# Optimization experiments

Hardware: AMD Instinct MI355X
Metric: run time of the kernel (lower is better)

Reference implementation:

```python
import jax, jax.numpy as jnp
import numpy as np

N = 96            # max_nodes == R (all nodes real)
IN_DIM, HID, ZD = 64, 256, 64
E = 1024
U = N * (N - 1) // 2
NUM_LOGITS = U + N   # 4656
MPM_ITERS = 50
BN_EPS = 1e-5

def _xavier_relu(k, fi, fo):
    # xavier_uniform with gain('relu') = sqrt(2)
    s = (2.0 ** 0.5) * (6.0 / (fi + fo)) ** 0.5
    return jax.random.uniform(k, (fi, fo), jnp.float32, -s, s)

def setup_inputs() -> dict:
    key = jax.random.key(0)
    ks = jax.random.split(key, 12)
    x = jax.random.normal(ks[0], (N, IN_DIM), jnp.float32)
    edge_index = jnp.stack([jax.random.randint(ks[1], (E,), 0, N),
                            jax.random.randint(ks[2], (E,), 0, N)]).astype(jnp.int32)
    a = (jax.random.uniform(ks[3], (N, N)) < 0.06).astype(jnp.float32)
    adj_gt = jnp.maximum(a, a.T) * (1.0 - jnp.eye(N, dtype=jnp.float32))
    return dict(
        x=x, edge_index=edge_index, adj_gt=adj_gt,
        W1=_xavier_relu(ks[4], IN_DIM, HID), b1=jnp.zeros(HID, jnp.float32),
        gamma1=jnp.ones(HID, jnp.float32), beta1=jnp.zeros(HID, jnp.float32),
        W2=_xavier_relu(ks[5], HID, HID), b2=jnp.zeros(HID, jnp.float32),
        gamma2=jnp.ones(HID, jnp.float32), beta2=jnp.zeros(HID, jnp.float32),
        Wmu=_xavier_relu(ks[6], HID, ZD), bmu=jnp.zeros(ZD, jnp.float32),
        Wlv=_xavier_relu(ks[7], HID, ZD), blv=jnp.zeros(ZD, jnp.float32),
        Wd1=_xavier_relu(ks[8], ZD, HID), bd1=jnp.zeros(HID, jnp.float32),
        Wd2=_xavier_relu(ks[9], HID, NUM_LOGITS), bd2=jnp.zeros(NUM_LOGITS, jnp.float32),
        eps=jax.random.normal(ks[10], (ZD,), jnp.float32))

def _bn(h, g, b):
    # BatchNorm1d, training mode: normalize over nodes (axis 0)
    m = h.mean(0)
    v = h.var(0)
    return (h - m) * jax.lax.rsqrt(v + BN_EPS) * g + b

def _forward(x, adj_gt, W1, b1, gamma1, beta1, W2, b2, gamma2, beta2,
             Wmu, bmu, Wlv, blv, Wd1, bd1, Wd2, bd2, eps, edge_index):
    ar = jnp.arange(N)
    eye = jnp.eye(N, dtype=bool)
    A = jnp.zeros((N, N), jnp.float32).at[edge_index[0], edge_index[1]].set(1.0)
    A = jnp.maximum(A, jnp.eye(N, dtype=jnp.float32))  # self loops
    dinv = jax.lax.rsqrt(A.sum(1))
    A_norm = A * dinv[:, None] * dinv[None, :]
    h = jax.nn.relu(_bn(A_norm @ (x @ W1) + b1, gamma1, beta1))
    h = jax.nn.relu(_bn(A_norm @ (h @ W2) + b2, gamma2, beta2))
    # ---- readout, reparam, decode ----
    g_vec = h.sum(0) / N                      # divide by real node count R
    mu = g_vec @ Wmu + bmu
    lv = jnp.clip(g_vec @ Wlv + blv, -4.0, 4.0)
    z = mu + eps * jnp.exp(0.5 * lv)
    vec = jnp.tanh(jax.nn.relu(z @ Wd1 + bd1) @ Wd2 + bd2)  # [NUM_LOGITS]
    # ---- vec_to_adj ----
    iu = jnp.triu_indices(N, 1)
    Ah = jnp.zeros((N, N), jnp.float32).at[iu].set(vec[:U])
    Ah = (Ah + Ah.T).at[ar, ar].set(vec[U:])  # adjacency logits
    # ---- edge similarity tensor S[i,j,a,b] ----
    Agt = adj_gt.at[ar, ar].set(1.0)
    B = jax.nn.sigmoid(Ah).at[ar, ar].set(1.0)
    degA, degB = Agt.sum(1), B.sum(1)
    node_sim = 1.0 / (jnp.abs(degA[:, None] - degB[None, :]) + 1.0)  # [N,N]
    dA, dB = jnp.diag(Agt), jnp.diag(B)
    S = (Agt[:, :, None, None] * dA[:, None, None, None] * dA[None, :, None, None]
         * B[None, None, :, :] * dB[None, None, :, None] * dB[None, None, None, :])
    xor = eye[:, :, None, None] ^ eye[None, None, :, :]
    S = jnp.where(xor, 0.0, S)
    diag_val = dA[:, None] * dB[None, :] * node_sim  # value at (i,i,a,a)
    both = eye[:, :, None, None] & eye[None, None, :, :]
    S = jnp.where(both, diag_val[:, None, :, None], S)
    # ---- MPM iteration (fixed 50 steps) ----
    nd = S[ar[:, None], ar[:, None], ar[None, :], ar[None, :]]  # node sim [N,N]
    offmask = (~eye)[:, :, None].astype(S.dtype)                # [N,N,1] over (i,j)
    def step(X, _):
        node_term = X * nd
        XS_max = (S * X[None, :, None, :]).max(-1)  # (i,j,a): max_b X[j,b]*S[i,j,a,b]
        edge_term = (XS_max * offmask).sum(1)       # sum over j != i
        Xn = node_term + edge_term
        Xn = Xn / jnp.linalg.norm(Xn)               # Frobenius norm
        return Xn, None
    X0 = jnp.full((N, N), 1.0 / N, jnp.float32)
    X, _ = jax.lax.scan(jax.checkpoint(step), X0, None, length=MPM_ITERS)
    return X

def reference(x, edge_index, adj_gt, W1, b1, gamma1, beta1, W2, b2, gamma2, beta2,
              Wmu, bmu, Wlv, blv, Wd1, bd1, Wd2, bd2, eps):
    return _forward(x, adj_gt, W1, b1, gamma1, beta1, W2, b2, gamma2, beta2,
                    Wmu, bmu, Wlv, blv, Wd1, bd1, Wd2, bd2, eps, edge_index)
```

## Files before the change

kernel.cpp:

```cpp
#include <hip/hip_runtime.h>
#include <math.h>

#define NN    96
#define EE    1024
#define HID   256
#define IND   64
#define ZD    64
#define NL    4656
#define NBLK  96
#define NTHR  384
#define ITERS 50
#define NBARS 8
#define SHF   (HID*49)

typedef unsigned long long ull;

struct Params {
  const float* x; const int* ei; const float* adj;
  const float* W1; const float* b1; const float* g1; const float* be1;
  const float* W2; const float* b2; const float* g2; const float* be2;
  const float* Wmu; const float* bmu; const float* Wlv; const float* blv;
  const float* Wd1; const float* bd1; const float* Wd2; const float* bd2;
  const float* eps; float* out;
};

__device__ float d_XW[NN*HID];
__device__ float d_H1pre[NN*HID];
__device__ float d_HW2[NN*HID];
__device__ float d_H2pre[NN*HID];
__device__ float d_mean1[HID], d_istd1[HID];
__device__ float d_gvec[HID];
__device__ float d_vec[NL];
__device__ float d_P[2][NN*NN];
__device__ ull   d_prog[2][NN];
__device__ float d_rssq[NN];
__device__ int   d_flag[NBLK];
__device__ int   d_rel;
__device__ int   d_epoch;

__device__ __forceinline__ float gld(const float* p) {
  return __hip_atomic_load(p, __ATOMIC_RELAXED, __HIP_MEMORY_SCOPE_AGENT);
}
__device__ __forceinline__ void gst(float* p, float v) {
  __hip_atomic_store(p, v, __ATOMIC_RELAXED, __HIP_MEMORY_SCOPE_AGENT);
}
__device__ __forceinline__ ull ldp(const ull* p) {
  return __hip_atomic_load(p, __ATOMIC_RELAXED, __HIP_MEMORY_SCOPE_AGENT);
}
__device__ __forceinline__ void stp(ull* p, ull v) {
  __hip_atomic_store(p, v, __ATOMIC_RELAXED, __HIP_MEMORY_SCOPE_AGENT);
}

__device__ __forceinline__ float wsum(float v) {
  v += __shfl_xor(v, 32, 64);
  v += __shfl_xor(v, 16, 64);
  v += __shfl_xor(v,  8, 64);
  v += __shfl_xor(v,  4, 64);
  v += __shfl_xor(v,  2, 64);
  v += __shfl_xor(v,  1, 64);
  return v;
}
__device__ __forceinline__ float wmax(float v) {
  v = fmaxf(v, __shfl_xor(v, 32, 64));
  v = fmaxf(v, __shfl_xor(v, 16, 64));
  v = fmaxf(v, __shfl_xor(v,  8, 64));
  v = fmaxf(v, __shfl_xor(v,  4, 64));
  v = fmaxf(v, __shfl_xor(v,  2, 64));
  v = fmaxf(v, __shfl_xor(v,  1, 64));
  return v;
}

__device__ __forceinline__ int tri_idx(int a, int c) {
  return a*95 - (a*(a-1))/2 + (c - a - 1);
}

__device__ __forceinline__ void gbar(int idx, int base) {
  asm volatile("s_waitcnt vmcnt(0)" ::: "memory");
  __syncthreads();
  const int tgt = base + idx + 1;
  const int t = threadIdx.x;
  if (blockIdx.x == 0) {
    if (t >= 1 && t < NBLK) {
      while (__hip_atomic_load(&d_flag[t], __ATOMIC_RELAXED, __HIP_MEMORY_SCOPE_AGENT) < tgt)
        __builtin_amdgcn_s_sleep(1);
    }
    __syncthreads();
    if (t == 0)
      __hip_atomic_store(&d_rel, tgt, __ATOMIC_RELAXED, __HIP_MEMORY_SCOPE_AGENT);
  } else {
    if (t == 0) {
      __hip_atomic_store(&d_flag[blockIdx.x], tgt, __ATOMIC_RELAXED, __HIP_MEMORY_SCOPE_AGENT);
      while (__hip_atomic_load(&d_rel, __ATOMIC_RELAXED, __HIP_MEMORY_SCOPE_AGENT) < tgt)
        __builtin_amdgcn_s_sleep(1);
    }
    __syncthreads();
  }
}

__global__ void __launch_bounds__(NTHR) gvae_kernel(Params p) {
  const int b = blockIdx.x;
  const int t = threadIdx.x;

  __shared__ __align__(16) float SH[SHF];
  __shared__ float pre1[HID];
  __shared__ float sg[HID], sd1[HID], sz[ZD];
  __shared__ float dinv[NN];
  __shared__ float eV[NN];   __shared__ int eL[NN];  __shared__ int s_ecnt;
  __shared__ float ndrow[NN], rowsq[NN], xb2[NN];
  __shared__ int   nbrL[NN];
  __shared__ int   s_dE[NN];
  __shared__ float sdegA;    __shared__ int s_cnt;
  __shared__ float sF;       __shared__ int s_ei;  __shared__ int s_emax;

  const int epoch = __hip_atomic_load(&d_epoch, __ATOMIC_RELAXED, __HIP_MEMORY_SCOPE_AGENT);
  const int base  = epoch * NBARS;
  const ull ep64  = (ull)epoch * 64ull;

  for (int i = t; i < NN*97; i += NTHR) SH[i] = 0.0f;
  __syncthreads();
  for (int e = t; e < EE; e += NTHR) {
    int s = p.ei[e], d = p.ei[EE + e];
    SH[s*97 + d] = 1.0f;
  }
  if (t < NN) SH[t*97 + t] = 1.0f;
  __syncthreads();
  if (t < NN) {
    float s = 0.0f;
    for (int j = 0; j < NN; ++j) s += SH[t*97 + j];
    dinv[t] = 1.0f / sqrtf(s);
  }
  if (t < 64) {
    bool is1 = SH[b*97 + t] > 0.5f;
    ull m1 = __ballot(is1);
    if (is1) eL[__popcll(m1 & ((1ull << t) - 1))] = t;
    int c1 = __popcll(m1);
    bool is2 = (t < 32) && SH[b*97 + 64 + t] > 0.5f;
    ull m2 = __ballot(is2);
    if (is2) eL[c1 + __popcll(m2 & ((1ull << t) - 1))] = 64 + t;
    if (t == 0) s_ecnt = c1 + __popcll(m2);
  }
  __syncthreads();
  if (t < s_ecnt) eV[t] = dinv[b] * dinv[eL[t]];
  if (t < HID) {
    float acc = 0.0f;
    for (int d = 0; d < IND; ++d) acc += p.x[b*IND + d] * p.W1[d*HID + t];
    gst(&d_XW[b*HID + t], acc);
  }
  gbar(0, base);

  {
    const int lim = s_ecnt * HID;
    float tv[16];
    #pragma unroll
    for (int r = 0; r < 16; ++r) {
      int idx = t + r*NTHR;
      if (idx < lim) tv[r] = gld(&d_XW[eL[idx >> 8]*HID + (idx & 255)]);
    }
    #pragma unroll
    for (int r = 0; r < 16; ++r) {
      int idx = t + r*NTHR;
      if (idx < lim) SH[idx] = tv[r];
    }
    for (int idx = t + 16*NTHR; idx < lim; idx += NTHR)
      SH[idx] = gld(&d_XW[eL[idx >> 8]*HID + (idx & 255)]);
    __syncthreads();
    if (t < HID) {
      float acc = 0.0f;
      const int ec = s_ecnt;
      for (int n = 0; n < ec; ++n) acc += eV[n] * SH[n*HID + t];
      acc += p.b1[t];
      pre1[t] = acc;
      gst(&d_H1pre[b*HID + t], acc);
    }
  }
  gbar(1, base);

  if (b < 86) {
    int w = t >> 6, lane = t & 63;
    int c = b*3 + w;
    if (w < 3 && c < HID) {
      float v0 = gld(&d_H1pre[lane*HID + c]);
      float v1 = (lane < 32) ? gld(&d_H1pre[(64+lane)*HID + c]) : 0.0f;
      float mean = wsum(v0 + v1) * (1.0f/96.0f);
      float a0 = v0 - mean, a1 = (lane < 32) ? (v1 - mean) : 0.0f;
      float var = wsum(a0*a0 + a1*a1) * (1.0f/96.0f);
      if (lane == 0) { gst(&d_mean1[c], mean); gst(&d_istd1[c], 1.0f/sqrtf(var + 1e-5f)); }
    }
  }
  gbar(2, base);

  if (t < HID) {
    float m = gld(&d_mean1[t]), is = gld(&d_istd1[t]);
    pre1[t] = fmaxf((pre1[t] - m) * is * p.g1[t] + p.be1[t], 0.0f);
  }
  __syncthreads();
  if (t < HID) {
    float acc = 0.0f;
    for (int k = 0; k < HID; ++k) acc += pre1[k] * p.W2[k*HID + t];
    gst(&d_HW2[b*HID + t], acc);
  }
  gbar(3, base);

  {
    const int lim = s_ecnt * HID;
    float tv[16];
    #pragma unroll
    for (int r = 0; r < 16; ++r) {
      int idx = t + r*NTHR;
      if (idx < lim) tv[r] = gld(&d_HW2[eL[idx >> 8]*HID + (idx & 255)]);
    }
    #pragma unroll
    for (int r = 0; r < 16; ++r) {
      int idx = t + r*NTHR;
      if (idx < lim) SH[idx] = tv[r];
    }
    for (int idx = t + 16*NTHR; idx < lim; idx += NTHR)
      SH[idx] = gld(&d_HW2[eL[idx >> 8]*HID + (idx & 255)]);
    __syncthreads();
    if (t < HID) {
      float acc = 0.0f;
      const int ec = s_ecnt;
      for (int n = 0; n < ec; ++n) acc += eV[n] * SH[n*HID + t];
      acc += p.b2[t];
      gst(&d_H2pre[b*HID + t], acc);
    }
  }
  gbar(4, base);

  if (b < 86) {
    int w = t >> 6, lane = t & 63;
    int c = b*3 + w;
    if (w < 3 && c < HID) {
      float v0 = gld(&d_H2pre[lane*HID + c]);
      float v1 = (lane < 32) ? gld(&d_H2pre[(64+lane)*HID + c]) : 0.0f;
      float mean = wsum(v0 + v1) * (1.0f/96.0f);
      float a0 = v0 - mean, a1 = (lane < 32) ? (v1 - mean) : 0.0f;
      float var = wsum(a0*a0 + a1*a1) * (1.0f/96.0f);
      float is = 1.0f / sqrtf(var + 1e-5f);
      float ga = p.g2[c], be = p.be2[c];
      float h0 = fmaxf((v0 - mean)*is*ga + be, 0.0f);
      float h1v = (lane < 32) ? fmaxf((v1 - mean)*is*ga + be, 0.0f) : 0.0f;
      float gs = wsum(h0 + h1v);
      if (lane == 0) gst(&d_gvec[c], gs * (1.0f/96.0f));
    }
  }
  gbar(5, base);

  if (t < HID) sg[t] = gld(&d_gvec[t]);
  __syncthreads();
  if (t < ZD) {
    float am = p.bmu[t], al = p.blv[t];
    for (int c = 0; c < HID; ++c) {
      float gv = sg[c];
      am += gv * p.Wmu[c*ZD + t];
      al += gv * p.Wlv[c*ZD + t];
    }
    al = fminf(fmaxf(al, -4.0f), 4.0f);
    sz[t] = am + p.eps[t] * expf(0.5f * al);
  }
  __syncthreads();
  if (t < HID) {
    float acc = p.bd1[t];
    for (int d = 0; d < ZD; ++d) acc += sz[d] * p.Wd1[d*HID + t];
    sd1[t] = fmaxf(acc, 0.0f);
  }
  __syncthreads();
  {
    const int o0 = b*49;
    const int nout = min(49, NL - o0);
    #pragma unroll 4
    for (int idx = t; idx < HID*49; idx += NTHR) {
      int k = idx / 49, o = idx - k*49;
      SH[idx] = (o0 + o < NL) ? p.Wd2[k*NL + o0 + o] : 0.0f;
    }
    __syncthreads();
    if (t < nout) {
      float acc = p.bd2[o0 + t];
      for (int k = 0; k < HID; ++k) acc += sd1[k] * SH[k*49 + t];
      gst(&d_vec[o0 + t], tanhf(acc));
    }
  }
  gbar(6, base);

  {
    float tv[13];
    #pragma unroll
    for (int r = 0; r < 13; ++r) {
      int idx = t + r*NTHR;
      if (idx < NL) tv[r] = gld(&d_vec[idx]);
    }
    #pragma unroll
    for (int r = 0; r < 13; ++r) {
      int idx = t + r*NTHR;
      if (idx < NL) SH[idx] = tv[r];
    }
  }
  const int kk = t >> 2;
  const int qq = t & 3;
  if (t < 64) {
    float s = p.adj[b*NN + t] + ((t < 32) ? p.adj[b*NN + 64 + t] : 0.0f);
    s = wsum(s);
    if (t == 0) sdegA = s + 1.0f;
    bool is1 = (t != b) && (p.adj[b*NN + t] > 0.5f);
    ull m1 = __ballot(is1);
    if (is1) nbrL[__popcll(m1 & ((1ull << t) - 1))] = t;
    int c1 = __popcll(m1);
    bool is2 = (t < 32) && ((64 + t) != b) && (p.adj[b*NN + 64 + t] > 0.5f);
    ull m2 = __ballot(is2);
    if (is2) nbrL[c1 + __popcll(m2 & ((1ull << t) - 1))] = 64 + t;
    if (t == 0) s_cnt = c1 + __popcll(m2);
  }
  __syncthreads();

  float breg[24];
  {
    float bs = 0.0f;
    const int lb = qq*24;
    #pragma unroll
    for (int s = 0; s < 24; ++s) {
      int l = lb + s;
      float v = 0.0f;
      if (l != kk) {
        int a  = kk < l ? kk : l;
        int cc = kk < l ? l : kk;
        v = 1.0f / (1.0f + expf(-SH[tri_idx(a, cc)]));
      }
      breg[s] = v;
      bs += v;
    }
    float tot = bs + __shfl_xor(bs, 1, 64);
    tot += __shfl_xor(tot, 2, 64);
    if (qq == 0) ndrow[kk] = 1.0f / (fabsf(sdegA - (tot + 1.0f)) + 1.0f);
  }
  __syncthreads();

  const int cnt = s_cnt;
  int E_own = 0;

  {
    float vm = 0.0f;
    #pragma unroll
    for (int s = 0; s < 24; ++s) vm = fmaxf(vm, breg[s] * (1.0f/96.0f));
    vm = fmaxf(vm, __shfl_xor(vm, 1, 64));
    vm = fmaxf(vm, __shfl_xor(vm, 2, 64));
    float acc = 0.0f;
    for (int n = 0; n < cnt; ++n) acc += vm;
    if (qq == 0) xb2[kk] = (1.0f/96.0f) * ndrow[kk] + acc;
  }
  __syncthreads();
  if (t < 64) {
    float m = xb2[t];
    if (t < 32) m = fmaxf(m, xb2[64 + t]);
    m = wmax(m);
    if (t == 0) s_ei = ilogbf(m);
  }
  __syncthreads();
  E_own += s_ei;
  if (qq == 0) {
    float Pv = ldexpf(xb2[kk], -s_ei);
    xb2[kk] = Pv;
    gst(&d_P[1][b*NN + kk], Pv);
  }
  asm volatile("s_waitcnt vmcnt(0)" ::: "memory");
  __syncthreads();
  if (t == 0) stp(&d_prog[1][b], ((ep64 + 1ull) << 16) | (ull)(E_own & 0xFFFF));

  for (int it = 2; it <= ITERS; ++it) {
    const int pb = (it - 1) & 1;
    if (t < cnt) {
      const int j = nbrL[t];
      const ull want = ep64 + (ull)(it - 1);
      ull f;
      while (((f = ldp(&d_prog[pb][j])) >> 16) < want)
        __builtin_amdgcn_s_sleep(1);
      s_dE[t] = (int)(short)(f & 0xFFFF) - E_own;
    }
    __syncthreads();
    const int lim = cnt * NN;
    {
      float tv[8]; int te[8];
      #pragma unroll
      for (int r = 0; r < 8; ++r) {
        int idx = t + r*NTHR;
        if (idx < lim) {
          int slot = idx / NN, col = idx - slot*NN;
          tv[r] = gld(&d_P[pb][nbrL[slot]*NN + col]);
          te[r] = s_dE[slot];
        }
      }
      #pragma unroll
      for (int r = 0; r < 8; ++r) {
        int idx = t + r*NTHR;
        if (idx < lim) SH[idx] = ldexpf(tv[r], te[r]);
      }
      for (int idx = t + 8*NTHR; idx < lim; idx += NTHR) {
        int slot = idx / NN, col = idx - slot*NN;
        SH[idx] = ldexpf(gld(&d_P[pb][nbrL[slot]*NN + col]), s_dE[slot]);
      }
    }
    __syncthreads();
    float acc = 0.0f;
    for (int n = 0; n < cnt; ++n) {
      const float4* xp = reinterpret_cast<const float4*>(&SH[n*NN + qq*24]);
      float vm = 0.0f;
      #pragma unroll
      for (int s6 = 0; s6 < 6; ++s6) {
        float4 xv = xp[s6];
        vm = fmaxf(vm, breg[4*s6+0] * xv.x);
        vm = fmaxf(vm, breg[4*s6+1] * xv.y);
        vm = fmaxf(vm, breg[4*s6+2] * xv.z);
        vm = fmaxf(vm, breg[4*s6+3] * xv.w);
      }
      vm = fmaxf(vm, __shfl_xor(vm, 1, 64));
      vm = fmaxf(vm, __shfl_xor(vm, 2, 64));
      acc += vm;
    }
    if (qq == 0) xb2[kk] = xb2[kk] * ndrow[kk] + acc;
    __syncthreads();
    if (t < 64) {
      float m = xb2[t];
      if (t < 32) m = fmaxf(m, xb2[64 + t]);
      m = wmax(m);
      if (t == 0) s_ei = ilogbf(m);
    }
    __syncthreads();
    E_own += s_ei;
    if (qq == 0) {
      float Pv = ldexpf(xb2[kk], -s_ei);
      xb2[kk] = Pv;
      gst(&d_P[it & 1][b*NN + kk], Pv);
    }
    asm volatile("s_waitcnt vmcnt(0)" ::: "memory");
    __syncthreads();
    if (t == 0) stp(&d_prog[it & 1][b], ((ep64 + (ull)it) << 16) | (ull)(E_own & 0xFFFF));
  }

  if (t < NN) rowsq[t] = xb2[t] * xb2[t];
  __syncthreads();
  if (t < 64) {
    float v = rowsq[t] + ((t < 32) ? rowsq[64 + t] : 0.0f);
    v = wsum(v);
    if (t == 0) gst(&d_rssq[b], v);
  }
  gbar(7, base);
  if (t < NN) {
    ull f = ldp(&d_prog[ITERS & 1][t]);
    s_dE[t] = (int)(short)(f & 0xFFFF);
    rowsq[t] = gld(&d_rssq[t]);
  }
  __syncthreads();
  if (t == 0) {
    int em = s_dE[0];
    for (int j = 1; j < NN; ++j) em = max(em, s_dE[j]);
    float s = 0.0f;
    for (int j = 0; j < NN; ++j) s += ldexpf(rowsq[j], 2*(s_dE[j] - em));
    s_emax = em;
    sF = 1.0f / sqrtf(s);
  }
  __syncthreads();
  if (t < NN) p.out[b*NN + t] = ldexpf(xb2[t] * sF, E_own - s_emax);

  if (b == 0 && t == 0)
    __hip_atomic_fetch_add(&d_epoch, 1, __ATOMIC_RELAXED, __HIP_MEMORY_SCOPE_AGENT);
}

extern "C" void kernel_launch(void* const* d_in, const int* in_sizes, int n_in,
                              void* d_out, int out_size, void* d_ws, size_t ws_size,
                              hipStream_t stream) {
  Params prm;
  prm.x   = (const float*)d_in[0];
  prm.ei  = (const int*  )d_in[1];
  prm.adj = (const float*)d_in[2];
  prm.W1  = (const float*)d_in[3];
  prm.b1  = (const float*)d_in[4];
  prm.g1  = (const float*)d_in[5];
  prm.be1 = (const float*)d_in[6];
  prm.W2  = (const float*)d_in[7];
  prm.b2  = (const float*)d_in[8];
  prm.g2  = (const float*)d_in[9];
  prm.be2 = (const float*)d_in[10];
  prm.Wmu = (const float*)d_in[11];
  prm.bmu = (const float*)d_in[12];
  prm.Wlv = (const float*)d_in[13];
  prm.blv = (const float*)d_in[14];
  prm.Wd1 = (const float*)d_in[15];
  prm.bd1 = (const float*)d_in[16];
  prm.Wd2 = (const float*)d_in[17];
  prm.bd2 = (const float*)d_in[18];
  prm.eps = (const float*)d_in[19];
  prm.out = (float*)d_out;

  gvae_kernel<<<dim3(NBLK), dim3(NTHR), 0, stream>>>(prm);
}
```

Measured before the change: 459.1 us.

## Replace per-block progress flags with epoch-tagged data words for MPM exchange

Each published P value now travels with its epoch tag and exponent in a pair of 64-bit words. Consumers poll the data itself and use a block-wide AND vote to confirm every word is current. This removes the separate flag spin, the vmcnt(0) drain and one barrier per iteration from the critical path between producer and consumer blocks. In exchange the exchanged data is four times wider (16 bytes per element instead of 4), and the whole neighbour tile must be re-polled until every tag matches.

```diff
diff --git a/kernel.cpp b/kernel.cpp
--- a/kernel.cpp
+++ b/kernel.cpp
@@ -31,8 +31,7 @@
 __device__ float d_mean1[HID], d_istd1[HID];
 __device__ float d_gvec[HID];
 __device__ float d_vec[NL];
-__device__ float d_P[2][NN*NN];
-__device__ ull   d_prog[2][NN];
+__device__ ulonglong2 d_Pw[2][NN*NN];
 __device__ float d_rssq[NN];
 __device__ int   d_flag[NBLK];
 __device__ int   d_rel;
@@ -356,47 +355,61 @@
   }
   __syncthreads();
   E_own += s_ei;
-  if (qq == 0) {
-    float Pv = ldexpf(xb2[kk], -s_ei);
-    xb2[kk] = Pv;
-    gst(&d_P[1][b*NN + kk], Pv);
-  }
-  asm volatile("s_waitcnt vmcnt(0)" ::: "memory");
-  __syncthreads();
-  if (t == 0) stp(&d_prog[1][b], ((ep64 + 1ull) << 16) | (ull)(E_own & 0xFFFF));
+  {
+    const ull tagw = (ep64 + 1ull) << 32;
+    if (qq == 0) {
+      float Pv = ldexpf(xb2[kk], -s_ei);
+      xb2[kk] = Pv;
+      stp(&d_Pw[1][b*NN + kk].x, tagw | (ull)(unsigned)E_own);
+      stp(&d_Pw[1][b*NN + kk].y, tagw | (ull)__float_as_uint(Pv));
+    }
+  }
 
   for (int it = 2; it <= ITERS; ++it) {
     const int pb = (it - 1) & 1;
-    if (t < cnt) {
-      const int j = nbrL[t];
-      const ull want = ep64 + (ull)(it - 1);
-      ull f;
-      while (((f = ldp(&d_prog[pb][j])) >> 16) < want)
-        __builtin_amdgcn_s_sleep(1);
-      s_dE[t] = (int)(short)(f & 0xFFFF) - E_own;
-    }
-    __syncthreads();
+    const ull want = ep64 + (ull)(it - 1);
     const int lim = cnt * NN;
-    {
-      float tv[8]; int te[8];
+    ull wa[8], wb[8];
+    for (;;) {
       #pragma unroll
       for (int r = 0; r < 8; ++r) {
         int idx = t + r*NTHR;
         if (idx < lim) {
           int slot = idx / NN, col = idx - slot*NN;
-          tv[r] = gld(&d_P[pb][nbrL[slot]*NN + col]);
-          te[r] = s_dE[slot];
+          const ulonglong2* wp = &d_Pw[pb][nbrL[slot]*NN + col];
+          wa[r] = ldp(&wp->x);
+          wb[r] = ldp(&wp->y);
         }
       }
+      int ok = 1;
       #pragma unroll
       for (int r = 0; r < 8; ++r) {
         int idx = t + r*NTHR;
-        if (idx < lim) SH[idx] = ldexpf(tv[r], te[r]);
+        if (idx < lim) ok &= ((wa[r] >> 32) == want) && ((wb[r] >> 32) == want);
       }
-      for (int idx = t + 8*NTHR; idx < lim; idx += NTHR) {
-        int slot = idx / NN, col = idx - slot*NN;
-        SH[idx] = ldexpf(gld(&d_P[pb][nbrL[slot]*NN + col]), s_dE[slot]);
+      if (__syncthreads_and(ok)) break;
+      __builtin_amdgcn_s_sleep(1);
+    }
+    #pragma unroll
+    for (int r = 0; r < 8; ++r) {
+      int idx = t + r*NTHR;
+      if (idx < lim) {
+        int Ej = (int)(unsigned)(wa[r] & 0xFFFFFFFFull);
+        float v = __uint_as_float((unsigned)(wb[r] & 0xFFFFFFFFull));
+        SH[idx] = ldexpf(v, Ej - E_own);
       }
+    }
+    for (int idx = t + 8*NTHR; idx < lim; idx += NTHR) {
+      int slot = idx / NN, col = idx - slot*NN;
+      const ulonglong2* wp = &d_Pw[pb][nbrL[slot]*NN + col];
+      ull A, B;
+      do {
+        A = ldp(&wp->x); B = ldp(&wp->y);
+        if (((A >> 32) == want) && ((B >> 32) == want)) break;
+        __builtin_amdgcn_s_sleep(1);
+      } while (true);
+      SH[idx] = ldexpf(__uint_as_float((unsigned)(B & 0xFFFFFFFFull)),
+                       (int)(unsigned)(A & 0xFFFFFFFFull) - E_own);
     }
     __syncthreads();
     float acc = 0.0f;
@@ -425,14 +438,15 @@
     }
     __syncthreads();
     E_own += s_ei;
-    if (qq == 0) {
-      float Pv = ldexpf(xb2[kk], -s_ei);
-      xb2[kk] = Pv;
-      gst(&d_P[it & 1][b*NN + kk], Pv);
-    }
-    asm volatile("s_waitcnt vmcnt(0)" ::: "memory");
-    __syncthreads();
-    if (t == 0) stp(&d_prog[it & 1][b], ((ep64 + (ull)it) << 16) | (ull)(E_own & 0xFFFF));
+    {
+      const ull tagw = (ep64 + (ull)it) << 32;
+      if (qq == 0) {
+        float Pv = ldexpf(xb2[kk], -s_ei);
+        xb2[kk] = Pv;
+        stp(&d_Pw[it & 1][b*NN + kk].x, tagw | (ull)(unsigned)E_own);
+        stp(&d_Pw[it & 1][b*NN + kk].y, tagw | (ull)__float_as_uint(Pv));
+      }
+    }
   }
 
   if (t < NN) rowsq[t] = xb2[t] * xb2[t];
@@ -444,8 +458,8 @@
   }
   gbar(7, base);
   if (t < NN) {
-    ull f = ldp(&d_prog[ITERS & 1][t]);
-    s_dE[t] = (int)(short)(f & 0xFFFF);
+    ull A = ldp(&d_Pw[ITERS & 1][t*NN].x);
+    s_dE[t] = (int)(unsigned)(A & 0xFFFFFFFFull);
     rowsq[t] = gld(&d_rssq[t]);
   }
   __syncthreads();
```

New measurement: 449.2 us. 1.02x faster.
